# Kernel tuning notes

Hardware: AMD Instinct MI355X
Metric: run time of the kernel (lower is better)

The kernel has to match this reference:

```python
import jax, jax.numpy as jnp
import numpy as np

NH = 25            # nHidden
NS = 20            # nStep (MPC horizon)
DT = 1.0 / 60.0    # del_t
EPS = 1e-4
PQ = 5.0           # terminal cost weight
QV = 200.0         # velocity cost weight
QA = 1.0           # control cost weight
BATCH = 131072
D = NH + 2         # augmented state dim


def setup_inputs() -> dict:
    key = jax.random.key(0)
    k1, k2, k3, k4, k5 = jax.random.split(key, 5)
    x = jax.random.normal(k1, (BATCH, NH), jnp.float32)
    gripper_p = jax.random.normal(k2, (BATCH,), jnp.float32)
    gripper_v = jax.random.normal(k3, (BATCH,), jnp.float32)
    # learned parameters of the module
    Af = jax.random.uniform(k4, (NH, 1), jnp.float32)               # feature->position coupling column
    Lq = jnp.tril(jax.random.uniform(k5, (NH, NH), jnp.float32))    # Cholesky-style factor of Q0
    return {"x": x, "gripper_p": gripper_p, "gripper_v": gripper_v, "Af": Af, "Lq": Lq}


def _build_system(Af, Lq):
    """Assemble the (batch-shared) MPC matrices: Q_final, p_final, S_, T_."""
    eyeD = jnp.eye(D, dtype=Af.dtype)
    # A0 = [[I, 0, Af], [0 .. 0, [1 dt; 0 1]]]
    top = jnp.concatenate([jnp.eye(NH, dtype=Af.dtype), jnp.zeros((NH, 1), Af.dtype), Af], axis=1)
    ap = jnp.concatenate([jnp.zeros((2, NH), Af.dtype),
                          jnp.array([[1.0, DT], [0.0, 1.0]], Af.dtype)], axis=1)
    A0 = jnp.concatenate([top, ap], axis=0)                                   # [D, D]
    B0 = jnp.concatenate([jnp.zeros((NH, 1), Af.dtype),
                          jnp.array([[0.5 * DT * DT], [DT]], Af.dtype)], axis=0)  # [D, 1]
    # stage cost Q0 (padded with [0 0; 0 Qv] block)
    Q0 = Lq @ Lq.T + EPS * jnp.eye(NH, dtype=Af.dtype)
    Q0f = (jnp.zeros((D, D), Af.dtype)
           .at[:NH, :NH].set(Q0)
           .at[NH:, NH:].set(jnp.array([[0.0, 0.0], [0.0, QV]], Af.dtype)))
    # powers A0^0..A0^NS (small fixed loop, NS=20)
    pows = [eyeD]
    for _ in range(NS):
        pows.append(pows[-1] @ A0)
    P = jnp.stack(pows)                    # [NS+1, D, D]
    T_ = P[1:].reshape(NS * D, D)          # stacked A0^1..A0^NS
    # S_ block (r,c) = A0^(r-c) @ B0 for c<=r (block lower-triangular), else 0
    SB = P @ B0                            # [NS+1, D, 1]
    r = jnp.arange(NS)
    diff = r[:, None] - r[None, :]         # [NS, NS]
    Sblk = jnp.where((diff >= 0)[:, :, None, None], SB[jnp.clip(diff, 0)], 0.0)  # [NS, NS, D, 1]
    S_ = Sblk.transpose(0, 2, 1, 3).reshape(NS * D, NS)
    # block-diagonal Q (last block scaled by Pq)
    Qblocks = jnp.concatenate([jnp.tile(Q0f[None], (NS - 1, 1, 1)), PQ * Q0f[None]], axis=0)
    Qd = jnp.zeros((NS, D, NS, D), Af.dtype).at[r, :, r, :].set(Qblocks).reshape(NS * D, NS * D)
    QS = Qd @ S_                                                       # [NS*D, NS]
    Q_final = 2.0 * (QA * jnp.eye(NS, dtype=Af.dtype) + S_.T @ QS) + EPS * jnp.eye(NS, dtype=Af.dtype)
    p_final = 2.0 * (T_.T @ QS)                                        # [D, NS]
    return Q_final, p_final, S_, T_


def reference(x, gripper_p, gripper_v, Af, Lq):
    nB = x.shape[0]
    Q_final, p_final, S_, T_ = _build_system(Af, Lq)
    x0 = jnp.concatenate([x, gripper_p[:, None], gripper_v[:, None]], axis=1)  # [B, D]
    p = x0 @ p_final                                                           # [B, NS]
    # QP with G=0, h=0 (trivially satisfied) and no equality constraints ->
    # unconstrained minimizer: u = -Q_final^{-1} p
    u = -jnp.linalg.solve(Q_final, p.T).T                                      # [B, NS]
    x_predict = u @ S_.T + x0 @ T_.T                                           # [B, NS*D]
    # output selector picks the gripper position entry (index NH) of each block
    return x_predict.reshape(nB, NS, D)[:, :, NH]                              # [B, NS]
```

## Files before the change

kernel.cpp:

```cpp
#include <hip/hip_runtime.h>

#define NHID 25
#define NSTEP 20
#define DT_ (1.0f/60.0f)
#define EPS_ 1e-4f
#define PQ_ 5.0f
#define QV_ 200.0f
#define QA_ 1.0f

__global__ __launch_bounds__(256) void mpc_fused(
    const float* __restrict__ x, const float* __restrict__ gp,
    const float* __restrict__ gv, const float* __restrict__ Af,
    const float* __restrict__ Lq, float* __restrict__ out)
{
    __shared__ float xs[256 * NHID];
    __shared__ float Lqs[NHID * NHID];
    __shared__ float Afs[NHID];
    __shared__ float wv_[NHID];
    __shared__ float us[NHID];
    __shared__ float alpha_s;
    __shared__ float zsh[2][NSTEP];
    __shared__ float bs[NSTEP];
    __shared__ float gs[NSTEP];

    const int t = threadIdx.x;
    const size_t b0 = (size_t)blockIdx.x * 256;
    const float dt = DT_;

    if (t < NHID) Afs[t] = Af[t];
    for (int i = t; i < NHID * NHID; i += 256) Lqs[i] = Lq[i];
    {
        const float4* xsrc = (const float4*)(x + b0 * NHID);
        float4* xdst = (float4*)xs;
        #pragma unroll
        for (int i = 0; i < 7; ++i) {
            int idx = t + 256 * i;
            if (idx < 1600) xdst[idx] = xsrc[idx];
        }
    }
    const float p = gp[b0 + t];
    const float v = gv[b0 + t];
    __syncthreads();

    if (t < NHID) {
        float acc = 0.0f;
        for (int i = t; i < NHID; ++i)
            acc = fmaf(Lqs[i * NHID + t], Afs[i], acc);
        wv_[t] = acc;
    }
    __syncthreads();
    if (t < NHID) {
        float acc = EPS_ * Afs[t];
        for (int j = 0; j <= t; ++j)
            acc = fmaf(Lqs[t * NHID + j], wv_[j], acc);
        us[t] = acc;
    }
    __syncthreads();
    if (t == 0) {
        float a = 0.0f;
        for (int i = 0; i < NHID; ++i) a = fmaf(Afs[i], us[i], a);
        alpha_s = a;
    }
    __syncthreads();

    if (t < 64) {
        const float alpha = alpha_s;
        float row[NSTEP + 2];
        #pragma unroll
        for (int c = 0; c < NSTEP; ++c) {
            int m0 = (t > c) ? t : c;
            float s = 0.0f;
            for (int rr = m0; rr < NSTEP; ++rr) {
                float wr = (rr == NSTEP - 1) ? PQ_ : 1.0f;
                s = fmaf(wr, fmaf((float)(rr - t) * (float)(rr - c), alpha, QV_), s);
            }
            row[c] = 2.0f * dt * dt * s + ((t == c) ? (2.0f * QA_ + EPS_) : 0.0f);
        }
        {
            float s20 = 0.0f, s21 = 0.0f;
            for (int rr = t; rr < NSTEP; ++rr) {
                float wr = (rr == NSTEP - 1) ? PQ_ : 1.0f;
                s20 += wr * (float)(rr - t);
                s21 = fmaf(wr, fmaf((float)(rr + 1) * (float)(rr - t), alpha, QV_), s21);
            }
            row[NSTEP]     = s20;
            row[NSTEP + 1] = s21;
        }
        #pragma unroll
        for (int piv = 0; piv < NSTEP; ++piv) {
            float pr[NSTEP + 2];
            #pragma unroll
            for (int c = piv; c < NSTEP + 2; ++c)
                pr[c] = __shfl(row[c], piv, 64);
            __builtin_amdgcn_sched_barrier(0);
            float pinv = 1.0f / pr[piv];
            float f = row[piv] * pinv;
            #pragma unroll
            for (int c = piv; c < NSTEP + 2; ++c) {
                float nv = fmaf(-f, pr[c], row[c]);
                row[c] = (t == piv) ? (pr[c] * pinv) : nv;
            }
        }
        if (t < NSTEP) { zsh[0][t] = row[NSTEP]; zsh[1][t] = row[NSTEP + 1]; }
    }
    __syncthreads();

    if (t < NSTEP) {
        const float hdt2 = 0.5f * dt * dt;
        float bacc = 0.0f, gacc = 0.0f;
        for (int c = 0; c <= t; ++c) {
            float ssel = fmaf((float)(t - c), dt * dt, hdt2);
            bacc = fmaf(zsh[0][c], ssel, bacc);
            gacc = fmaf(zsh[1][c], ssel, gacc);
        }
        bs[t] = -2.0f * dt * bacc;
        gs[t] = fmaf((float)(t + 1), dt, -2.0f * dt * gacc);
    }
    __syncthreads();

    const float* xr = xs + t * NHID;
    float tb = 0.0f;
    #pragma unroll
    for (int i = 0; i < NHID; ++i)
        tb = fmaf(xr[i], us[i], tb);

    float4* o4 = (float4*)(out + (b0 + t) * NSTEP);
    #pragma unroll
    for (int q = 0; q < 5; ++q) {
        float4 r;
        r.x = fmaf(tb, bs[4*q+0], fmaf(v, gs[4*q+0], p));
        r.y = fmaf(tb, bs[4*q+1], fmaf(v, gs[4*q+1], p));
        r.z = fmaf(tb, bs[4*q+2], fmaf(v, gs[4*q+2], p));
        r.w = fmaf(tb, bs[4*q+3], fmaf(v, gs[4*q+3], p));
        o4[q] = r;
    }
}

extern "C" void kernel_launch(void* const* d_in, const int* in_sizes, int n_in,
                              void* d_out, int out_size, void* d_ws, size_t ws_size,
                              hipStream_t stream) {
    const float* x  = (const float*)d_in[0];
    const float* gp = (const float*)d_in[1];
    const float* gv = (const float*)d_in[2];
    const float* Af = (const float*)d_in[3];
    const float* Lq = (const float*)d_in[4];
    float* out = (float*)d_out;

    const int B = in_sizes[1];
    hipLaunchKernelGGL(mpc_fused, dim3(B / 256), dim3(256), 0, stream,
                       x, gp, gv, Af, Lq, out);
}
```

Measured before the change: 90.28 us.

## Parallelize per-block Gauss-Jordan solve across all threads via shared memory

Replaces the single-wavefront register/shuffle Gauss-Jordan elimination of the 20x22 augmented system with a block-wide version. Every thread builds matrix entries into shared memory and updates up to two elements per pivot. The aim is to shorten the serial solve prologue each block runs before streaming its outputs. The cost is two block-wide barriers per pivot and extra shared-memory traffic.

After: 86.66 us. 1.04x faster.

```diff
diff --git a/kernel.cpp b/kernel.cpp
--- a/kernel.cpp
+++ b/kernel.cpp
@@ -7,6 +7,8 @@
 #define PQ_ 5.0f
 #define QV_ 200.0f
 #define QA_ 1.0f
+#define NAUG (NSTEP + 2)
+#define NEL  (NSTEP * NAUG)
 
 __global__ __launch_bounds__(256) void mpc_fused(
     const float* __restrict__ x, const float* __restrict__ gp,
@@ -19,7 +21,7 @@
     __shared__ float wv_[NHID];
     __shared__ float us[NHID];
     __shared__ float alpha_s;
-    __shared__ float zsh[2][NSTEP];
+    __shared__ float aug[NSTEP][NAUG + 2];
     __shared__ float bs[NSTEP];
     __shared__ float gs[NSTEP];
 
@@ -62,56 +64,63 @@
         alpha_s = a;
     }
     __syncthreads();
+    const float alpha = alpha_s;
 
-    if (t < 64) {
-        const float alpha = alpha_s;
-        float row[NSTEP + 2];
-        #pragma unroll
-        for (int c = 0; c < NSTEP; ++c) {
-            int m0 = (t > c) ? t : c;
+    for (int idx = t; idx < NEL; idx += 256) {
+        int r = idx / NAUG, c = idx % NAUG;
+        float val;
+        if (c < NSTEP) {
+            int m0 = (r > c) ? r : c;
             float s = 0.0f;
             for (int rr = m0; rr < NSTEP; ++rr) {
                 float wr = (rr == NSTEP - 1) ? PQ_ : 1.0f;
-                s = fmaf(wr, fmaf((float)(rr - t) * (float)(rr - c), alpha, QV_), s);
+                s = fmaf(wr, fmaf((float)(rr - r) * (float)(rr - c), alpha, QV_), s);
             }
-            row[c] = 2.0f * dt * dt * s + ((t == c) ? (2.0f * QA_ + EPS_) : 0.0f);
+            val = 2.0f * dt * dt * s + ((r == c) ? (2.0f * QA_ + EPS_) : 0.0f);
+        } else if (c == NSTEP) {
+            float s = 0.0f;
+            for (int rr = r; rr < NSTEP; ++rr)
+                s += ((rr == NSTEP - 1) ? PQ_ : 1.0f) * (float)(rr - r);
+            val = s;
+        } else {
+            float s = 0.0f;
+            for (int rr = r; rr < NSTEP; ++rr) {
+                float wr = (rr == NSTEP - 1) ? PQ_ : 1.0f;
+                s = fmaf(wr, fmaf((float)(rr + 1) * (float)(rr - r), alpha, QV_), s);
+            }
+            val = s;
         }
-        {
-            float s20 = 0.0f, s21 = 0.0f;
-            for (int rr = t; rr < NSTEP; ++rr) {
-                float wr = (rr == NSTEP - 1) ? PQ_ : 1.0f;
-                s20 += wr * (float)(rr - t);
-                s21 = fmaf(wr, fmaf((float)(rr + 1) * (float)(rr - t), alpha, QV_), s21);
-            }
-            row[NSTEP]     = s20;
-            row[NSTEP + 1] = s21;
-        }
-        #pragma unroll
-        for (int piv = 0; piv < NSTEP; ++piv) {
-            float pr[NSTEP + 2];
-            #pragma unroll
-            for (int c = piv; c < NSTEP + 2; ++c)
-                pr[c] = __shfl(row[c], piv, 64);
-            __builtin_amdgcn_sched_barrier(0);
-            float pinv = 1.0f / pr[piv];
-            float f = row[piv] * pinv;
-            #pragma unroll
-            for (int c = piv; c < NSTEP + 2; ++c) {
-                float nv = fmaf(-f, pr[c], row[c]);
-                row[c] = (t == piv) ? (pr[c] * pinv) : nv;
-            }
-        }
-        if (t < NSTEP) { zsh[0][t] = row[NSTEP]; zsh[1][t] = row[NSTEP + 1]; }
+        aug[r][c] = val;
     }
     __syncthreads();
+
+    const int r0 = t / NAUG,        c0 = t % NAUG;
+    const int r1 = (t + 256) / NAUG, c1 = (t + 256) % NAUG;
+    for (int piv = 0; piv < NSTEP; ++piv) {
+        float app  = aug[piv][piv];
+        float pinv = 1.0f / app;
+        float n0 = 0.0f, n1 = 0.0f;
+        if (t < NEL) {
+            float arc = aug[r0][c0], apc = aug[piv][c0], arp = aug[r0][piv];
+            n0 = (r0 == piv) ? arc * pinv : fmaf(-arp * pinv, apc, arc);
+        }
+        if (t < NEL - 256) {
+            float arc = aug[r1][c1], apc = aug[piv][c1], arp = aug[r1][piv];
+            n1 = (r1 == piv) ? arc * pinv : fmaf(-arp * pinv, apc, arc);
+        }
+        __syncthreads();
+        if (t < NEL)       aug[r0][c0] = n0;
+        if (t < NEL - 256) aug[r1][c1] = n1;
+        __syncthreads();
+    }
 
     if (t < NSTEP) {
         const float hdt2 = 0.5f * dt * dt;
         float bacc = 0.0f, gacc = 0.0f;
         for (int c = 0; c <= t; ++c) {
             float ssel = fmaf((float)(t - c), dt * dt, hdt2);
-            bacc = fmaf(zsh[0][c], ssel, bacc);
-            gacc = fmaf(zsh[1][c], ssel, gacc);
+            bacc = fmaf(aug[c][NSTEP],     ssel, bacc);
+            gacc = fmaf(aug[c][NSTEP + 1], ssel, gacc);
         }
         bs[t] = -2.0f * dt * bacc;
         gs[t] = fmaf((float)(t + 1), dt, -2.0f * dt * gacc);
```
